# Kernel tuning notes

Measured on AMD Instinct MI355X. Metric: run time of the kernel, lower is better.

## Reference

```python
import jax, jax.numpy as jnp
import numpy as np

SIGMA_D = 1.0  # init kwarg sigma_d
# d_model = 2 -> div_term = exp(arange(0,2,2) * (-ln(10000)/2)) = [1.0]


def setup_inputs() -> dict:
    key = jax.random.key(0)
    k0, k1 = jax.random.split(key)
    B, N, M = 4, 3000, 3000
    points0 = jax.random.normal(k0, (B, N, 2), dtype=jnp.float32)
    points1 = jax.random.normal(k1, (B, M, 2), dtype=jnp.float32)
    return {"points0": points0, "points1": points1}


def reference(points0, points1):
    # pairwise distance with points_normlize=True: sq_dist = clamp(2 - 2*<p0,p1>, 0)
    xy = jnp.einsum('bnc,bmc->bnm', points0, points1)  # (B,N,M)
    sq_dist = jnp.clip(2.0 - 2.0 * xy, 0.0)
    d_indices = jnp.sqrt(sq_dist) / SIGMA_D  # (B,N,M)
    # sinusoidal embedding with d_model=2, div_term=[1.0] -> [sin(d), cos(d)]
    d_embeddings = jnp.stack([jnp.sin(d_indices), jnp.cos(d_indices)], axis=-1)  # (B,N,M,2)
    d_embeddings = jax.lax.stop_gradient(d_embeddings)  # torch detaches + no_grad
    # einsum 'bnc,bnmc->bnc': multiply by sum over m
    points0_emb = points0 * d_embeddings.sum(axis=2)  # (B,N,2)
    # einsum 'bmc,bmnc->bmc' with permuted emb: sum over n
    points1_emb = points1 * d_embeddings.sum(axis=1)  # (B,M,2)
    return (points0_emb, points1_emb)
```

## Files before the change

### kernel.cpp

```cpp
#include <hip/hip_runtime.h>
#include <math.h>


#define GB 4
#define GN 3000
#define RB 16
#define BLKS 188
#define HALF 1500
#define K2 0.025330295910584444f
#define C2 0.050660591821168888f

#define COLPART_F2 (GB*BLKS*GN)

__device__ __forceinline__ float sreg(float x) {
    return __int_as_float(__builtin_amdgcn_readfirstlane(__float_as_int(x)));
}

__global__ __launch_bounds__(256, 6) void geo_pair_kernel(
    const float* __restrict__ p0,
    const float* __restrict__ p1,
    float2* __restrict__ ws)
{
    __shared__ float2 cp[4][768];

    const int lane = threadIdx.x & 63;
    const int wv   = threadIdx.x >> 6;
    const int h    = blockIdx.x & 1;
    const int t    = blockIdx.x >> 1;
    const int b    = t / BLKS;
    const int blk  = t - b * BLKS;
    const int row0 = blk * RB + wv * 4;
    const bool active = (row0 < GN);

    float s0=0.f,c0=0.f,s1=0.f,c1=0.f,s2=0.f,c2=0.f,s3=0.f,c3=0.f;
    float ax0=0.f,ay0=0.f,ax1=0.f,ay1=0.f,ax2=0.f,ay2=0.f,ax3=0.f,ay3=0.f;
    float2 pr0=make_float2(0.f,0.f), pr1=pr0, pr2=pr0, pr3=pr0;
    const float2* __restrict__ qp = (const float2*)p1;
    float2 qA = make_float2(0.f,0.f), qB = qA;
    const float c2v = C2;

    if (active) {
        const float2* ownp = (const float2*)p0 + b * GN + row0;
        pr0 = ownp[0]; pr1 = ownp[1]; pr2 = ownp[2]; pr3 = ownp[3];
        const float mm = -2.0f * K2;
        ax0 = sreg(mm * pr0.x); ay0 = sreg(mm * pr0.y);
        ax1 = sreg(mm * pr1.x); ay1 = sreg(mm * pr1.y);
        ax2 = sreg(mm * pr2.x); ay2 = sreg(mm * pr2.y);
        ax3 = sreg(mm * pr3.x); ay3 = sreg(mm * pr3.y);
        qp = (const float2*)p1 + b * GN + h * HALF + lane;
        qA = qp[0];
        qB = qp[64];
    } else {
        for (int i = lane; i < 768; i += 64)
            cp[wv][i] = make_float2(0.f, 0.f);
    }

    float2* cw = &cp[wv][lane];

#define STEP(q) do {                                                         \
    float t0 = fmaf(ax0, (q).x, fmaf(ay0, (q).y, c2v));                      \
    float t1 = fmaf(ax1, (q).x, fmaf(ay1, (q).y, c2v));                      \
    float t2 = fmaf(ax2, (q).x, fmaf(ay2, (q).y, c2v));                      \
    float t3 = fmaf(ax3, (q).x, fmaf(ay3, (q).y, c2v));                      \
    t0 = fmaxf(t0, 0.f); t1 = fmaxf(t1, 0.f);                                \
    t2 = fmaxf(t2, 0.f); t3 = fmaxf(t3, 0.f);                                \
    float r0 = __builtin_amdgcn_sqrtf(t0);                                   \
    float r1 = __builtin_amdgcn_sqrtf(t1);                                   \
    float r2 = __builtin_amdgcn_sqrtf(t2);                                   \
    float r3 = __builtin_amdgcn_sqrtf(t3);                                   \
    float sn0 = __builtin_amdgcn_sinf(r0), cs0 = __builtin_amdgcn_cosf(r0);  \
    float sn1 = __builtin_amdgcn_sinf(r1), cs1 = __builtin_amdgcn_cosf(r1);  \
    float sn2 = __builtin_amdgcn_sinf(r2), cs2 = __builtin_amdgcn_cosf(r2);  \
    float sn3 = __builtin_amdgcn_sinf(r3), cs3 = __builtin_amdgcn_cosf(r3);  \
    s0 += sn0; c0 += cs0; s1 += sn1; c1 += cs1;                              \
    s2 += sn2; c2 += cs2; s3 += sn3; c3 += cs3;                              \
    cw[0] = make_float2((sn0 + sn1) + (sn2 + sn3),                           \
                        (cs0 + cs1) + (cs2 + cs3));                          \
    cw += 64;                                                                \
} while (0)

    if (active) {
        #pragma unroll 1
        for (int js = 0; js < 10; ++js) {
            float2 qC = qp[128];
            qp += 64;
            STEP(qA);
            qA = qB; qB = qC;
        }
        STEP(qA);
        STEP(qB);
        qA = qp[128];
        qB = qp[192];
        qp += 128;
    }
    __syncthreads();
    float2* __restrict__ dst = ws + (b * BLKS + blk) * GN + h * HALF;
    for (int i = threadIdx.x; i < 768; i += 256) {
        float2 a0 = cp[0][i], a1 = cp[1][i], a2 = cp[2][i], a3 = cp[3][i];
        dst[i] = make_float2((a0.x + a1.x) + (a2.x + a3.x),
                             (a0.y + a1.y) + (a2.y + a3.y));
    }
    __syncthreads();

    cw = &cp[wv][lane];
    if (active) {
        #pragma unroll 1
        for (int js = 0; js < 9; ++js) {
            float2 qC = qp[128];
            qp += 64;
            STEP(qA);
            qA = qB; qB = qC;
        }
        STEP(qA);
        STEP(qB);
        if (lane < 28) {
            float2 qT = qp[128];
            STEP(qT);
        }
    }
    __syncthreads();
    for (int i = threadIdx.x; i < 732; i += 256) {
        float2 a0 = cp[0][i], a1 = cp[1][i], a2 = cp[2][i], a3 = cp[3][i];
        dst[768 + i] = make_float2((a0.x + a1.x) + (a2.x + a3.x),
                                   (a0.y + a1.y) + (a2.y + a3.y));
    }
#undef STEP

    if (active) {
        #pragma unroll
        for (int off = 32; off >= 1; off >>= 1) {
            s0 += __shfl_down(s0, off, 64);  c0 += __shfl_down(c0, off, 64);
            s1 += __shfl_down(s1, off, 64);  c1 += __shfl_down(c1, off, 64);
            s2 += __shfl_down(s2, off, 64);  c2 += __shfl_down(c2, off, 64);
            s3 += __shfl_down(s3, off, 64);  c3 += __shfl_down(c3, off, 64);
        }
        if (lane == 0) {
            float2* rp = ws + COLPART_F2 + ((b * GN + row0) << 1) + h;
            rp[0] = make_float2(s0, c0);
            rp[2] = make_float2(s1, c1);
            rp[4] = make_float2(s2, c2);
            rp[6] = make_float2(s3, c3);
        }
    }
}

__global__ __launch_bounds__(256, 4) void geo_reduce_kernel(
    const float* __restrict__ p0,
    const float* __restrict__ p1,
    const float2* __restrict__ ws,
    float2* __restrict__ out)
{
    __shared__ float2 acc[8][32];
    const int blk = blockIdx.x;
    if (blk < 375) {
        const int c  = threadIdx.x & 31;
        const int kc = threadIdx.x >> 5;
        const int g  = blk * 32 + c;
        const int b  = g / GN;
        const int m  = g - b * GN;
        const float2* __restrict__ base = ws + b * (BLKS * GN) + m;
        const int k0 = kc * 24;
        float s = 0.f, cc = 0.f;
        #pragma unroll
        for (int j = 0; j < 24; ++j) {
            const int k = k0 + j;
            if (k < BLKS) {
                float2 v = base[k * GN];
                s += v.x; cc += v.y;
            }
        }
        acc[kc][c] = make_float2(s, cc);
        __syncthreads();
        if (kc == 0) {
            float2 r = acc[0][c];
            #pragma unroll
            for (int j = 1; j < 8; ++j) { r.x += acc[j][c].x; r.y += acc[j][c].y; }
            const float2 p = ((const float2*)p1)[g];
            out[GB * GN + g] = make_float2(p.x * r.x, p.y * r.y);
        }
    } else {
        const int r = (blk - 375) * 256 + threadIdx.x;
        if (r < GB * GN) {
            const float2* rp = ws + COLPART_F2 + (r << 1);
            const float2 a = rp[0], d = rp[1];
            const float2 p = ((const float2*)p0)[r];
            out[r] = make_float2(p.x * (a.x + d.x), p.y * (a.y + d.y));
        }
    }
}

extern "C" void kernel_launch(void* const* d_in, const int* in_sizes, int n_in,
                              void* d_out, int out_size, void* d_ws, size_t ws_size,
                              hipStream_t stream) {
    const float* points0 = (const float*)d_in[0];
    const float* points1 = (const float*)d_in[1];

    geo_pair_kernel<<<dim3(GB * BLKS * 2), dim3(256), 0, stream>>>(
        points0, points1, (float2*)d_ws);
    geo_reduce_kernel<<<dim3(375 + 47), dim3(256), 0, stream>>>(
        points0, points1, (const float2*)d_ws, (float2*)d_out);
}
```

Baseline: 85.85 us.

## Process eight rows per wave to halve column-partial workspace traffic

Each wavefront now handles 8 rows of points0 instead of 4, so a block covers 32 rows and the number of row-blocks drops from 188 to 94. This halves the column-partial sums written to the workspace and read back by the reduce kernel, and amortises each loaded points1 element over more transcendental evaluations. The cost is more registers per thread (launch bounds lowered from 6 to 4 blocks per SM), fewer blocks in the grid, and a longer per-step dependency chain.

Measured after the change: 80.51 us. 1.07x faster.

```diff
diff --git a/kernel.cpp b/kernel.cpp
--- a/kernel.cpp
+++ b/kernel.cpp
@@ -4,8 +4,8 @@
 
 #define GB 4
 #define GN 3000
-#define RB 16
-#define BLKS 188
+#define RB 32
+#define BLKS 94
 #define HALF 1500
 #define K2 0.025330295910584444f
 #define C2 0.050660591821168888f
@@ -16,7 +16,7 @@
     return __int_as_float(__builtin_amdgcn_readfirstlane(__float_as_int(x)));
 }
 
-__global__ __launch_bounds__(256, 6) void geo_pair_kernel(
+__global__ __launch_bounds__(256, 4) void geo_pair_kernel(
     const float* __restrict__ p0,
     const float* __restrict__ p1,
     float2* __restrict__ ws)
@@ -29,24 +29,29 @@
     const int t    = blockIdx.x >> 1;
     const int b    = t / BLKS;
     const int blk  = t - b * BLKS;
-    const int row0 = blk * RB + wv * 4;
+    const int row0 = blk * RB + wv * 8;
     const bool active = (row0 < GN);
 
-    float s0=0.f,c0=0.f,s1=0.f,c1=0.f,s2=0.f,c2=0.f,s3=0.f,c3=0.f;
-    float ax0=0.f,ay0=0.f,ax1=0.f,ay1=0.f,ax2=0.f,ay2=0.f,ax3=0.f,ay3=0.f;
-    float2 pr0=make_float2(0.f,0.f), pr1=pr0, pr2=pr0, pr3=pr0;
+    float s[8], c[8], ax[8], ay[8];
+    float2 pr[8];
+    #pragma unroll
+    for (int r = 0; r < 8; ++r) {
+        s[r] = 0.f; c[r] = 0.f; ax[r] = 0.f; ay[r] = 0.f;
+        pr[r] = make_float2(0.f, 0.f);
+    }
     const float2* __restrict__ qp = (const float2*)p1;
-    float2 qA = make_float2(0.f,0.f), qB = qA;
+    float2 qA = make_float2(0.f, 0.f), qB = qA;
     const float c2v = C2;
 
     if (active) {
         const float2* ownp = (const float2*)p0 + b * GN + row0;
-        pr0 = ownp[0]; pr1 = ownp[1]; pr2 = ownp[2]; pr3 = ownp[3];
         const float mm = -2.0f * K2;
-        ax0 = sreg(mm * pr0.x); ay0 = sreg(mm * pr0.y);
-        ax1 = sreg(mm * pr1.x); ay1 = sreg(mm * pr1.y);
-        ax2 = sreg(mm * pr2.x); ay2 = sreg(mm * pr2.y);
-        ax3 = sreg(mm * pr3.x); ay3 = sreg(mm * pr3.y);
+        #pragma unroll
+        for (int r = 0; r < 8; ++r) {
+            pr[r] = ownp[r];
+            ax[r] = sreg(mm * pr[r].x);
+            ay[r] = sreg(mm * pr[r].y);
+        }
         qp = (const float2*)p1 + b * GN + h * HALF + lane;
         qA = qp[0];
         qB = qp[64];
@@ -58,24 +63,21 @@
     float2* cw = &cp[wv][lane];
 
 #define STEP(q) do {                                                         \
-    float t0 = fmaf(ax0, (q).x, fmaf(ay0, (q).y, c2v));                      \
-    float t1 = fmaf(ax1, (q).x, fmaf(ay1, (q).y, c2v));                      \
-    float t2 = fmaf(ax2, (q).x, fmaf(ay2, (q).y, c2v));                      \
-    float t3 = fmaf(ax3, (q).x, fmaf(ay3, (q).y, c2v));                      \
-    t0 = fmaxf(t0, 0.f); t1 = fmaxf(t1, 0.f);                                \
-    t2 = fmaxf(t2, 0.f); t3 = fmaxf(t3, 0.f);                                \
-    float r0 = __builtin_amdgcn_sqrtf(t0);                                   \
-    float r1 = __builtin_amdgcn_sqrtf(t1);                                   \
-    float r2 = __builtin_amdgcn_sqrtf(t2);                                   \
-    float r3 = __builtin_amdgcn_sqrtf(t3);                                   \
-    float sn0 = __builtin_amdgcn_sinf(r0), cs0 = __builtin_amdgcn_cosf(r0);  \
-    float sn1 = __builtin_amdgcn_sinf(r1), cs1 = __builtin_amdgcn_cosf(r1);  \
-    float sn2 = __builtin_amdgcn_sinf(r2), cs2 = __builtin_amdgcn_cosf(r2);  \
-    float sn3 = __builtin_amdgcn_sinf(r3), cs3 = __builtin_amdgcn_cosf(r3);  \
-    s0 += sn0; c0 += cs0; s1 += sn1; c1 += cs1;                              \
-    s2 += sn2; c2 += cs2; s3 += sn3; c3 += cs3;                              \
-    cw[0] = make_float2((sn0 + sn1) + (sn2 + sn3),                           \
-                        (cs0 + cs1) + (cs2 + cs3));                          \
+    float sn[8], cs[8];                                                      \
+    _Pragma("unroll")                                                        \
+    for (int r = 0; r < 8; ++r) {                                            \
+        float tt = fmaf(ax[r], (q).x, fmaf(ay[r], (q).y, c2v));              \
+        tt = fmaxf(tt, 0.f);                                                 \
+        float rr = __builtin_amdgcn_sqrtf(tt);                               \
+        sn[r] = __builtin_amdgcn_sinf(rr);                                   \
+        cs[r] = __builtin_amdgcn_cosf(rr);                                   \
+        s[r] += sn[r]; c[r] += cs[r];                                        \
+    }                                                                        \
+    float ssum = ((sn[0]+sn[1]) + (sn[2]+sn[3]))                             \
+               + ((sn[4]+sn[5]) + (sn[6]+sn[7]));                            \
+    float csum = ((cs[0]+cs[1]) + (cs[2]+cs[3]))                             \
+               + ((cs[4]+cs[5]) + (cs[6]+cs[7]));                            \
+    cw[0] = make_float2(ssum, csum);                                         \
     cw += 64;                                                                \
 } while (0)
 
@@ -129,17 +131,17 @@
     if (active) {
         #pragma unroll
         for (int off = 32; off >= 1; off >>= 1) {
-            s0 += __shfl_down(s0, off, 64);  c0 += __shfl_down(c0, off, 64);
-            s1 += __shfl_down(s1, off, 64);  c1 += __shfl_down(c1, off, 64);
-            s2 += __shfl_down(s2, off, 64);  c2 += __shfl_down(c2, off, 64);
-            s3 += __shfl_down(s3, off, 64);  c3 += __shfl_down(c3, off, 64);
+            #pragma unroll
+            for (int r = 0; r < 8; ++r) {
+                s[r] += __shfl_down(s[r], off, 64);
+                c[r] += __shfl_down(c[r], off, 64);
+            }
         }
         if (lane == 0) {
             float2* rp = ws + COLPART_F2 + ((b * GN + row0) << 1) + h;
-            rp[0] = make_float2(s0, c0);
-            rp[2] = make_float2(s1, c1);
-            rp[4] = make_float2(s2, c2);
-            rp[6] = make_float2(s3, c3);
+            #pragma unroll
+            for (int r = 0; r < 8; ++r)
+                rp[r * 2] = make_float2(s[r], c[r]);
         }
     }
 }
@@ -153,28 +155,28 @@
     __shared__ float2 acc[8][32];
     const int blk = blockIdx.x;
     if (blk < 375) {
-        const int c  = threadIdx.x & 31;
+        const int cc = threadIdx.x & 31;
         const int kc = threadIdx.x >> 5;
-        const int g  = blk * 32 + c;
+        const int g  = blk * 32 + cc;
         const int b  = g / GN;
         const int m  = g - b * GN;
         const float2* __restrict__ base = ws + b * (BLKS * GN) + m;
-        const int k0 = kc * 24;
-        float s = 0.f, cc = 0.f;
+        const int k0 = kc * 12;
+        float sv = 0.f, cv = 0.f;
         #pragma unroll
-        for (int j = 0; j < 24; ++j) {
+        for (int j = 0; j < 12; ++j) {
             const int k = k0 + j;
             if (k < BLKS) {
                 float2 v = base[k * GN];
-                s += v.x; cc += v.y;
+                sv += v.x; cv += v.y;
             }
         }
-        acc[kc][c] = make_float2(s, cc);
+        acc[kc][cc] = make_float2(sv, cv);
         __syncthreads();
         if (kc == 0) {
-            float2 r = acc[0][c];
+            float2 r = acc[0][cc];
             #pragma unroll
-            for (int j = 1; j < 8; ++j) { r.x += acc[j][c].x; r.y += acc[j][c].y; }
+            for (int j = 1; j < 8; ++j) { r.x += acc[j][cc].x; r.y += acc[j][cc].y; }
             const float2 p = ((const float2*)p1)[g];
             out[GB * GN + g] = make_float2(p.x * r.x, p.y * r.y);
         }
```
